# Performance work log

Hardware: AMD Instinct MI355X
Metric: run time of the kernel (lower is better)

## Reference

```python
import jax, jax.numpy as jnp
import numpy as np

B, C, F_IN = 262144, 4, 4   # batch, num label nodes, feature dim
HID = 64                     # hidden_dim (MLP embedding dim / GCN input)
GCN_H, GCN_OUT = 32, 4
EPS = 1e-8                   # torch F.cosine_similarity eps


def _glorot(k, shape):
    lim = float(np.sqrt(6.0 / (shape[0] + shape[1])))
    return jax.random.uniform(k, shape, jnp.float32, -lim, lim)


def setup_inputs() -> dict:
    key = jax.random.key(0)
    ks = jax.random.split(key, 7)
    return dict(
        x=jax.random.normal(ks[0], (B, C, F_IN), jnp.float32),
        # LabelEmbeddingMLP: 4 -> 128 -> 64 -> HID
        W1=_glorot(ks[1], (F_IN, 128)), b1=jnp.zeros((128,), jnp.float32),
        W2=_glorot(ks[2], (128, 64)),   b2=jnp.zeros((64,), jnp.float32),
        W3=_glorot(ks[3], (64, HID)),   b3=jnp.zeros((HID,), jnp.float32),
        # GCNModel: GCNConv(HID,32) -> GCNConv(32,4)
        Wg1=_glorot(ks[4], (HID, GCN_H)), bg1=jnp.zeros((GCN_H,), jnp.float32),
        Wg2=_glorot(ks[5], (GCN_H, GCN_OUT)), bg2=jnp.zeros((GCN_OUT,), jnp.float32),
    )


def reference(x, W1, b1, W2, b2, W3, b3, Wg1, bg1, Wg2, bg2):
    # --- label embedding MLP (applied per node) ---
    h = jax.nn.relu(x @ W1 + b1)
    h = jax.nn.relu(h @ W2 + b2)
    emb = h @ W3 + b3                                    # [B, C, HID]

    # --- per-sample cosine similarity, thresholded, unioned over batch ---
    # (the torch code keeps adding edges to ONE nx.Graph across all k, so the
    #  resulting 4-node edge set is the union over the batch; edge weights are
    #  ignored because GCNConv is called without edge_weight)
    n = x / jnp.maximum(jnp.linalg.norm(x, axis=-1, keepdims=True), EPS)
    sim = jnp.einsum('bif,bjf->bij', n, n)               # [B, C, C]
    adj = (sim > 0.5).any(axis=0) & ~jnp.eye(C, dtype=bool)
    adj = adj | adj.T

    # --- GCN normalized adjacency with self-loops: D^-1/2 (A+I) D^-1/2 ---
    A = adj.astype(jnp.float32) + jnp.eye(C, dtype=jnp.float32)
    dinv = jax.lax.rsqrt(A.sum(axis=1))
    Ahat = jax.lax.stop_gradient(dinv[:, None] * A * dinv[None, :])  # graph built via .item() is detached in torch

    # --- two GCNConv layers, shared Ahat broadcast over batch ---
    g = jax.nn.relu(jnp.einsum('ij,bjh->bih', Ahat, emb @ Wg1) + bg1)  # [B, C, 32]
    out = jnp.einsum('ij,bjh->bih', Ahat, g @ Wg2) + bg2               # [B, C, 4]
    return emb, out
```

## Files before the change

kernel.cpp:

```cpp
#include <hip/hip_runtime.h>

#define NB 262144
#define NNODE (NB * 4)
#define EMB_ELEMS ((size_t)NNODE * 64)
#define ADJ_BLOCKS (NNODE / 256)

typedef __attribute__((ext_vector_type(8))) _Float16 f16x8;
typedef __attribute__((ext_vector_type(4))) float f32x4;
typedef __attribute__((ext_vector_type(4))) unsigned int u32x4;

#define OW1E  0
#define OW2T  10240
#define OW3T  27648
#define OW3GT 36864
#define OF32  41472
#define IMG_BYTES 42880
#define FB2   0
#define FB3   64
#define FB3G  128
#define FBG1  160
#define FWG2  192
#define FBG2  320
#define FAHAT 324

#define NWAVE 8
#define SB_STRIDE 36
#define WBUF_BYTES (64 * SB_STRIDE * 2)
#define SMEM_BYTES (IMG_BYTES + NWAVE * WBUF_BYTES)

__device__ __forceinline__ int kperm(int ji) {
    int kt = ji >> 5, r = ji & 31, g = r >> 3, e = r & 7;
    return kt * 32 + ((e >> 2) << 4) + (g << 2) + (e & 3);
}

template <int J>
__device__ __forceinline__ float qb(float v) {
    constexpr int ctrl = J | (J << 2) | (J << 4) | (J << 6);
    int r = __builtin_amdgcn_update_dpp(0, __builtin_bit_cast(int, v), ctrl, 0xF, 0xF, true);
    return __builtin_bit_cast(float, r);
}

__global__ __launch_bounds__(256) void adj_kernel(const float* __restrict__ x,
                                                  unsigned int* __restrict__ mask_arr) {
    __shared__ unsigned int smask;
    if (threadIdx.x == 0) smask = 0u;
    __syncthreads();

    const int t = blockIdx.x * 256 + threadIdx.x;
    const int c = t & 3;
    f32x4 v = *(const f32x4*)(x + (size_t)t * 4);
    float nn = sqrtf(v.x * v.x + v.y * v.y + v.z * v.z + v.w * v.w);
    float inv = 1.0f / fmaxf(nn, 1e-8f);

    unsigned int m = 0u;
#define DOTJ(J) do {                                                            \
        const float bx = qb<J>(v.x), by = qb<J>(v.y);                           \
        const float bz = qb<J>(v.z), bw = qb<J>(v.w);                           \
        const float bi = qb<J>(inv);                                            \
        const float d = v.x * bx + v.y * by + v.z * bz + v.w * bw;              \
        if ((int)((J) != c) & (int)(d * inv * bi > 0.5f)) {                     \
            const int i_ = c < (J) ? c : (J);                                   \
            const int j_ = c < (J) ? (J) : c;                                   \
            m |= 1u << (2 * i_ + j_ - 1 - (i_ >> 1));                           \
        }                                                                       \
    } while (0)
    DOTJ(0); DOTJ(1); DOTJ(2); DOTJ(3);
#undef DOTJ

    if (m) atomicOr(&smask, m);
    __syncthreads();
    if (threadIdx.x == 0) mask_arr[blockIdx.x] = smask;
}

__global__ __launch_bounds__(256) void prep_kernel(
    const float* __restrict__ W1, const float* __restrict__ b1,
    const float* __restrict__ W2, const float* __restrict__ b2,
    const float* __restrict__ W3, const float* __restrict__ b3,
    const float* __restrict__ Wg1, const float* __restrict__ bg1,
    const float* __restrict__ Wg2, const float* __restrict__ bg2,
    const unsigned int* __restrict__ mask_arr, char* __restrict__ img)
{
    const int t = threadIdx.x;
    const int bid = blockIdx.x;
    _Float16* H = (_Float16*)img;
    float* F = (float*)(img + OF32);

    if (bid == 0) {
        __shared__ unsigned red[256];
        unsigned um = 0u;
        for (int i = t; i < ADJ_BLOCKS; i += 256) um |= mask_arr[i];
        red[t] = um;
        __syncthreads();
        for (int s = 128; s > 0; s >>= 1) {
            if (t < s) red[t] |= red[t + s];
            __syncthreads();
        }
        const unsigned m = red[0];

        for (int i = t; i < 64; i += 256) F[FB2 + i] = b2[i];
        for (int i = t; i < 64; i += 256) F[FB3 + i] = b3[i];
        for (int i = t; i < 32; i += 256) {
            float s = 0.f;
            for (int h = 0; h < 64; ++h) s = fmaf(b3[h], Wg1[h * 32 + i], s);
            F[FB3G + i] = s;
        }
        for (int i = t; i < 32; i += 256) F[FBG1 + i] = bg1[i];
        for (int i = t; i < 128; i += 256) F[FWG2 + i] = Wg2[i];
        for (int i = t; i < 4; i += 256) F[FBG2 + i] = bg2[i];
        if (t == 0) {
            float A[4][4];
            for (int i = 0; i < 4; ++i)
                for (int j = 0; j < 4; ++j) A[i][j] = (i == j) ? 1.f : 0.f;
            int bit = 0;
            for (int i = 0; i < 4; ++i)
                for (int j = i + 1; j < 4; ++j) {
                    if ((m >> bit) & 1u) { A[i][j] = 1.f; A[j][i] = 1.f; }
                    ++bit;
                }
            float dinv[4];
            for (int i = 0; i < 4; ++i)
                dinv[i] = 1.0f / sqrtf(A[i][0] + A[i][1] + A[i][2] + A[i][3]);
            for (int i = 0; i < 4; ++i)
                for (int j = 0; j < 4; ++j) F[FAHAT + i * 4 + j] = dinv[i] * A[i][j] * dinv[j];
        }
    } else if (bid == 1) {
        for (int i = t; i < 128 * 40; i += 256) {
            int j = i / 40, kk = i % 40;
            float v = (kk < 4) ? W1[kk * 128 + j] : (kk == 4 ? b1[j] : 0.f);
            H[OW1E / 2 + i] = (_Float16)v;
        }
    } else if (bid == 2) {
        for (int i = t; i < 64 * 136; i += 256) {
            int jo = i / 136, ji = i % 136;
            float v = 0.f;
            if (ji < 128) v = W2[kperm(ji) * 64 + jo];
            H[OW2T / 2 + i] = (_Float16)v;
        }
    } else {
        for (int i = t; i < 64 * 72; i += 256) {
            int h = i / 72, j = i % 72;
            float v = 0.f;
            if (j < 64) v = W3[kperm(j) * 64 + h];
            H[OW3T / 2 + i] = (_Float16)v;
        }
        for (int i = t; i < 32 * 72; i += 256) {
            int e = i / 72, j = i % 72;
            float s = 0.f;
            if (j < 64) {
                const int jj = kperm(j);
                for (int h = 0; h < 64; ++h) s = fmaf(W3[jj * 64 + h], Wg1[h * 32 + e], s);
            }
            H[OW3GT / 2 + i] = (_Float16)s;
        }
    }
}

__device__ __forceinline__ unsigned pkf16(float a, float b) {
    unsigned short ha = __builtin_bit_cast(unsigned short, (_Float16)a);
    unsigned short hb = __builtin_bit_cast(unsigned short, (_Float16)b);
    return (unsigned)ha | ((unsigned)hb << 16);
}
__device__ __forceinline__ f32x4 MF(f16x8 a, f16x8 b, f32x4 c) {
    return __builtin_amdgcn_mfma_f32_16x16x32_f16(a, b, c, 0, 0, 0);
}
__device__ __forceinline__ f16x8 ldA(const _Float16* p) {
    return *(const f16x8*)p;
}
__device__ __forceinline__ f16x8 bcat(unsigned X0, unsigned X1,
                                      unsigned Y0, unsigned Y1) {
    u32x4 t; t.x = X0; t.y = X1; t.z = Y0; t.w = Y1;
    return __builtin_bit_cast(f16x8, t);
}

__global__ __launch_bounds__(512, 2) void mlp_gcn_mfma(
    const float* __restrict__ x, const char* __restrict__ img,
    float* __restrict__ emb_out, float* __restrict__ out_out)
{
    __shared__ u32x4 smem4[SMEM_BYTES / 16];
    char* smem = (char*)smem4;
    const int tx = threadIdx.x;
    {
        const u32x4* src = (const u32x4*)img;
        u32x4* dst = (u32x4*)smem;
        for (int i = tx; i < IMG_BYTES / 16; i += 512) dst[i] = src[i];
    }
    __syncthreads();

    const _Float16* wh = (const _Float16*)smem;
    const float* wf = (const float*)(smem + OF32);

    const int wid = tx >> 6, lane = tx & 63;
    const int g = lane >> 4, c = lane & 15;
    const bool g0 = (g == 0);

    char* wb = smem + IMG_BYTES + wid * WBUF_BYTES;
    _Float16* sb = (_Float16*)wb;
    float* tb = (float*)wb;

    const f32x4 arow = *(const f32x4*)(wf + FAHAT + (c & 3) * 4);
    f32x4 bg1v[2];
    bg1v[0] = *(const f32x4*)(wf + FBG1 + g * 4);
    bg1v[1] = *(const f32x4*)(wf + FBG1 + 16 + g * 4);
    const f32x4 bg2v = *(const f32x4*)(wf + FBG2);
    f32x4 wg2v[2][4];
#pragma unroll
    for (int m = 0; m < 2; ++m)
#pragma unroll
        for (int r = 0; r < 4; ++r)
            wg2v[m][r] = *(const f32x4*)(wf + FWG2 + (m * 16 + g * 4 + r) * 4);

    const size_t nbase0 = ((size_t)blockIdx.x * NWAVE + wid) * 128;
    f32x4 xv = *(const f32x4*)(x + (nbase0 + lane) * 4);

#pragma unroll 1
    for (int it = 0; it < 2; ++it) {
        const size_t nbase = nbase0 + (size_t)it * 64;
        const size_t pn = (it < 1) ? (nbase + 64) : nbase;
        f32x4 xnext = *(const f32x4*)(x + (pn + lane) * 4);

        {
            uint2 w0; w0.x = pkf16(xv.x, xv.y); w0.y = pkf16(xv.z, xv.w);
            uint2 w1; w1.x = 0x00003C00u; w1.y = 0u;
            *(uint2*)(sb + lane * SB_STRIDE + 0) = w0;
            *(uint2*)(sb + lane * SB_STRIDE + 4) = w1;
        }
        f16x8 xB[4];
#pragma unroll
        for (int nt = 0; nt < 4; ++nt) {
            uint2 lo = *(const uint2*)(sb + (nt * 16 + c) * SB_STRIDE + 0);
            uint2 hi = *(const uint2*)(sb + (nt * 16 + c) * SB_STRIDE + 4);
            u32x4 t;
            t.x = g0 ? lo.x : 0u; t.y = g0 ? lo.y : 0u;
            t.z = g0 ? hi.x : 0u; t.w = 0u;
            xB[nt] = __builtin_bit_cast(f16x8, t);
        }

        f32x4 acc2[4][4];
#pragma unroll
        for (int mt = 0; mt < 4; ++mt) {
            f32x4 bv = *(const f32x4*)(wf + FB2 + mt * 16 + g * 4);
#pragma unroll
            for (int nt = 0; nt < 4; ++nt) acc2[mt][nt] = bv;
        }
#pragma unroll
        for (int kt = 0; kt < 4; ++kt) {
            f16x8 a0 = ldA(wh + OW1E / 2 + ((2 * kt + 0) * 16 + c) * 40 + g * 8);
            f16x8 a1 = ldA(wh + OW1E / 2 + ((2 * kt + 1) * 16 + c) * 40 + g * 8);
            f16x8 bf[4];
#pragma unroll
            for (int nt = 0; nt < 4; ++nt) {
                f32x4 z = {0.f, 0.f, 0.f, 0.f};
                f32x4 t0 = MF(a0, xB[nt], z);
                f32x4 t1 = MF(a1, xB[nt], z);
                bf[nt] = bcat(pkf16(fmaxf(t0[0], 0.f), fmaxf(t0[1], 0.f)),
                              pkf16(fmaxf(t0[2], 0.f), fmaxf(t0[3], 0.f)),
                              pkf16(fmaxf(t1[0], 0.f), fmaxf(t1[1], 0.f)),
                              pkf16(fmaxf(t1[2], 0.f), fmaxf(t1[3], 0.f)));
            }
#pragma unroll
            for (int mt = 0; mt < 4; ++mt) {
                f16x8 a = ldA(wh + OW2T / 2 + (mt * 16 + c) * 136 + kt * 32 + g * 8);
#pragma unroll
                for (int nt = 0; nt < 4; ++nt) acc2[mt][nt] = MF(a, bf[nt], acc2[mt][nt]);
            }
        }

        unsigned pk2a[4][4][2];
#pragma unroll
        for (int mt = 0; mt < 4; ++mt)
#pragma unroll
            for (int nt = 0; nt < 4; ++nt) {
                pk2a[mt][nt][0] = pkf16(fmaxf(acc2[mt][nt][0], 0.f), fmaxf(acc2[mt][nt][1], 0.f));
                pk2a[mt][nt][1] = pkf16(fmaxf(acc2[mt][nt][2], 0.f), fmaxf(acc2[mt][nt][3], 0.f));
            }

        f32x4 acc3[4][4], acc4[2][4];
#pragma unroll
        for (int mt = 0; mt < 4; ++mt) {
            f32x4 bv = *(const f32x4*)(wf + FB3 + mt * 16 + g * 4);
#pragma unroll
            for (int nt = 0; nt < 4; ++nt) acc3[mt][nt] = bv;
        }
#pragma unroll
        for (int mt = 0; mt < 2; ++mt) {
            f32x4 bv = *(const f32x4*)(wf + FB3G + mt * 16 + g * 4);
#pragma unroll
            for (int nt = 0; nt < 4; ++nt) acc4[mt][nt] = bv;
        }
#pragma unroll
        for (int kt = 0; kt < 2; ++kt) {
            f16x8 bf[4];
#pragma unroll
            for (int nt = 0; nt < 4; ++nt)
                bf[nt] = bcat(pk2a[2 * kt][nt][0], pk2a[2 * kt][nt][1],
                              pk2a[2 * kt + 1][nt][0], pk2a[2 * kt + 1][nt][1]);
#pragma unroll
            for (int mt = 0; mt < 4; ++mt) {
                f16x8 a = ldA(wh + OW3T / 2 + (mt * 16 + c) * 72 + kt * 32 + g * 8);
#pragma unroll
                for (int nt = 0; nt < 4; ++nt) acc3[mt][nt] = MF(a, bf[nt], acc3[mt][nt]);
            }
#pragma unroll
            for (int mt = 0; mt < 2; ++mt) {
                f16x8 a = ldA(wh + OW3GT / 2 + (mt * 16 + c) * 72 + kt * 32 + g * 8);
#pragma unroll
                for (int nt = 0; nt < 4; ++nt) acc4[mt][nt] = MF(a, bf[nt], acc4[mt][nt]);
            }
        }

#pragma unroll
        for (int nt = 0; nt < 4; ++nt) {
#pragma unroll
            for (int mt = 0; mt < 4; ++mt) {
                int sl = (mt * 4 + g) ^ (c & 7);
                *(f32x4*)(tb + c * 64 + sl * 4) = acc3[mt][nt];
            }
            float* gp = emb_out + (nbase + nt * 16) * 64;
#pragma unroll
            for (int s = 0; s < 4; ++s) {
                int row = s * 4 + g;
                int sl = c ^ (row & 7);
                f32x4 q = *(const f32x4*)(tb + row * 64 + sl * 4);
                *(f32x4*)(gp + s * 256 + lane * 4) = q;
            }
        }

#pragma unroll
        for (int nt = 0; nt < 4; ++nt) {
            float u[4] = {0.f, 0.f, 0.f, 0.f};
#pragma unroll
            for (int m = 0; m < 2; ++m)
#pragma unroll
                for (int r = 0; r < 4; ++r) {
                    float v = acc4[m][nt][r];
                    float s = bg1v[m][r];
                    s = fmaf(arow.x, qb<0>(v), s);
                    s = fmaf(arow.y, qb<1>(v), s);
                    s = fmaf(arow.z, qb<2>(v), s);
                    s = fmaf(arow.w, qb<3>(v), s);
                    s = fmaxf(s, 0.f);
                    u[0] = fmaf(s, wg2v[m][r].x, u[0]);
                    u[1] = fmaf(s, wg2v[m][r].y, u[1]);
                    u[2] = fmaf(s, wg2v[m][r].z, u[2]);
                    u[3] = fmaf(s, wg2v[m][r].w, u[3]);
                }
#pragma unroll
            for (int o = 0; o < 4; ++o) {
                u[o] += __shfl_xor(u[o], 16);
                u[o] += __shfl_xor(u[o], 32);
            }
            float ov[4];
#pragma unroll
            for (int o = 0; o < 4; ++o) {
                float s = bg2v[o];
                s = fmaf(arow.x, qb<0>(u[o]), s);
                s = fmaf(arow.y, qb<1>(u[o]), s);
                s = fmaf(arow.z, qb<2>(u[o]), s);
                s = fmaf(arow.w, qb<3>(u[o]), s);
                ov[o] = s;
            }
            if (g0) {
                f32x4 t; t.x = ov[0]; t.y = ov[1]; t.z = ov[2]; t.w = ov[3];
                *(f32x4*)(out_out + (nbase + nt * 16 + c) * 4) = t;
            }
        }

        xv = xnext;
    }
}

extern "C" void kernel_launch(void* const* d_in, const int* in_sizes, int n_in,
                              void* d_out, int out_size, void* d_ws, size_t ws_size,
                              hipStream_t stream) {
    const float* x   = (const float*)d_in[0];
    const float* W1  = (const float*)d_in[1];
    const float* b1  = (const float*)d_in[2];
    const float* W2  = (const float*)d_in[3];
    const float* b2  = (const float*)d_in[4];
    const float* W3  = (const float*)d_in[5];
    const float* b3  = (const float*)d_in[6];
    const float* Wg1 = (const float*)d_in[7];
    const float* bg1 = (const float*)d_in[8];
    const float* Wg2 = (const float*)d_in[9];
    const float* bg2 = (const float*)d_in[10];

    unsigned int* mask_arr = (unsigned int*)d_ws;
    char* img = (char*)d_ws + 16640;

    float* emb_out = (float*)d_out;
    float* out_out = emb_out + EMB_ELEMS;

    adj_kernel<<<ADJ_BLOCKS, 256, 0, stream>>>(x, mask_arr);
    prep_kernel<<<4, 256, 0, stream>>>(W1, b1, W2, b2, W3, b3, Wg1, bg1, Wg2, bg2,
                                       mask_arr, img);
    mlp_gcn_mfma<<<NNODE / 1024, 512, 0, stream>>>(x, img, emb_out, out_out);
}
```

Measured before the change: 112.8 us.

## Compute GCN layer-2 projection with MFMA and load x directly into B fragments

Replaces the scalar FMA plus cross-lane shuffle reduction for the second GCN projection (32->4) with a single fp16 MFMA per tile, using a zero-padded, permuted Wg2 fragment precomputed into the shared weight image. The x input is now loaded straight from global memory into the MFMA B operand, dropping the LDS staging buffer and the software prefetch. The emb store loop is moved after the out computation, possibly shortening register live ranges. In exchange it adds fp16 rounding of the GCN hidden activations and gives up the explicit x prefetch.

```diff
diff --git a/kernel.cpp b/kernel.cpp
--- a/kernel.cpp
+++ b/kernel.cpp
@@ -13,19 +13,18 @@
 #define OW2T  10240
 #define OW3T  27648
 #define OW3GT 36864
-#define OF32  41472
-#define IMG_BYTES 42880
+#define OWG2A 41472
+#define OF32  42752
+#define IMG_BYTES 43600
 #define FB2   0
 #define FB3   64
 #define FB3G  128
 #define FBG1  160
-#define FWG2  192
-#define FBG2  320
-#define FAHAT 324
+#define FBG2  192
+#define FAHAT 196
 
 #define NWAVE 8
-#define SB_STRIDE 36
-#define WBUF_BYTES (64 * SB_STRIDE * 2)
+#define WBUF_BYTES 4096
 #define SMEM_BYTES (IMG_BYTES + NWAVE * WBUF_BYTES)
 
 __device__ __forceinline__ int kperm(int ji) {
@@ -105,8 +104,12 @@
             F[FB3G + i] = s;
         }
         for (int i = t; i < 32; i += 256) F[FBG1 + i] = bg1[i];
-        for (int i = t; i < 128; i += 256) F[FWG2 + i] = Wg2[i];
         for (int i = t; i < 4; i += 256) F[FBG2 + i] = bg2[i];
+        for (int i = t; i < 16 * 40; i += 256) {
+            int o = i / 40, ji = i % 40;
+            float v = (o < 4 && ji < 32) ? Wg2[kperm(ji) * 4 + o] : 0.f;
+            H[OWG2A / 2 + i] = (_Float16)v;
+        }
         if (t == 0) {
             float A[4][4];
             for (int i = 0; i < 4; ++i)
@@ -193,45 +196,30 @@
     const int g = lane >> 4, c = lane & 15;
     const bool g0 = (g == 0);
 
-    char* wb = smem + IMG_BYTES + wid * WBUF_BYTES;
-    _Float16* sb = (_Float16*)wb;
-    float* tb = (float*)wb;
+    float* tb = (float*)(smem + IMG_BYTES) + wid * 1024;
 
     const f32x4 arow = *(const f32x4*)(wf + FAHAT + (c & 3) * 4);
     f32x4 bg1v[2];
     bg1v[0] = *(const f32x4*)(wf + FBG1 + g * 4);
     bg1v[1] = *(const f32x4*)(wf + FBG1 + 16 + g * 4);
     const f32x4 bg2v = *(const f32x4*)(wf + FBG2);
-    f32x4 wg2v[2][4];
-#pragma unroll
-    for (int m = 0; m < 2; ++m)
-#pragma unroll
-        for (int r = 0; r < 4; ++r)
-            wg2v[m][r] = *(const f32x4*)(wf + FWG2 + (m * 16 + g * 4 + r) * 4);
+    const f16x8 aWg2 = ldA(wh + OWG2A / 2 + c * 40 + g * 8);
 
     const size_t nbase0 = ((size_t)blockIdx.x * NWAVE + wid) * 128;
-    f32x4 xv = *(const f32x4*)(x + (nbase0 + lane) * 4);
 
 #pragma unroll 1
     for (int it = 0; it < 2; ++it) {
         const size_t nbase = nbase0 + (size_t)it * 64;
-        const size_t pn = (it < 1) ? (nbase + 64) : nbase;
-        f32x4 xnext = *(const f32x4*)(x + (pn + lane) * 4);
-
-        {
-            uint2 w0; w0.x = pkf16(xv.x, xv.y); w0.y = pkf16(xv.z, xv.w);
-            uint2 w1; w1.x = 0x00003C00u; w1.y = 0u;
-            *(uint2*)(sb + lane * SB_STRIDE + 0) = w0;
-            *(uint2*)(sb + lane * SB_STRIDE + 4) = w1;
-        }
+
         f16x8 xB[4];
 #pragma unroll
         for (int nt = 0; nt < 4; ++nt) {
-            uint2 lo = *(const uint2*)(sb + (nt * 16 + c) * SB_STRIDE + 0);
-            uint2 hi = *(const uint2*)(sb + (nt * 16 + c) * SB_STRIDE + 4);
+            f32x4 xq = *(const f32x4*)(x + (nbase + nt * 16 + c) * 4);
             u32x4 t;
-            t.x = g0 ? lo.x : 0u; t.y = g0 ? lo.y : 0u;
-            t.z = g0 ? hi.x : 0u; t.w = 0u;
+            t.x = g0 ? pkf16(xq.x, xq.y) : 0u;
+            t.y = g0 ? pkf16(xq.z, xq.w) : 0u;
+            t.z = g0 ? 0x00003C00u : 0u;
+            t.w = 0u;
             xB[nt] = __builtin_bit_cast(f16x8, t);
         }
 
@@ -310,24 +298,7 @@
 
 #pragma unroll
         for (int nt = 0; nt < 4; ++nt) {
-#pragma unroll
-            for (int mt = 0; mt < 4; ++mt) {
-                int sl = (mt * 4 + g) ^ (c & 7);
-                *(f32x4*)(tb + c * 64 + sl * 4) = acc3[mt][nt];
-            }
-            float* gp = emb_out + (nbase + nt * 16) * 64;
-#pragma unroll
-            for (int s = 0; s < 4; ++s) {
-                int row = s * 4 + g;
-                int sl = c ^ (row & 7);
-                f32x4 q = *(const f32x4*)(tb + row * 64 + sl * 4);
-                *(f32x4*)(gp + s * 256 + lane * 4) = q;
-            }
-        }
-
-#pragma unroll
-        for (int nt = 0; nt < 4; ++nt) {
-            float u[4] = {0.f, 0.f, 0.f, 0.f};
+            float gv[2][4];
 #pragma unroll
             for (int m = 0; m < 2; ++m)
 #pragma unroll
@@ -338,25 +309,20 @@
                     s = fmaf(arow.y, qb<1>(v), s);
                     s = fmaf(arow.z, qb<2>(v), s);
                     s = fmaf(arow.w, qb<3>(v), s);
-                    s = fmaxf(s, 0.f);
-                    u[0] = fmaf(s, wg2v[m][r].x, u[0]);
-                    u[1] = fmaf(s, wg2v[m][r].y, u[1]);
-                    u[2] = fmaf(s, wg2v[m][r].z, u[2]);
-                    u[3] = fmaf(s, wg2v[m][r].w, u[3]);
+                    gv[m][r] = fmaxf(s, 0.f);
                 }
-#pragma unroll
-            for (int o = 0; o < 4; ++o) {
-                u[o] += __shfl_xor(u[o], 16);
-                u[o] += __shfl_xor(u[o], 32);
-            }
+            f16x8 bfg = bcat(pkf16(gv[0][0], gv[0][1]), pkf16(gv[0][2], gv[0][3]),
+                             pkf16(gv[1][0], gv[1][1]), pkf16(gv[1][2], gv[1][3]));
+            f32x4 z = {0.f, 0.f, 0.f, 0.f};
+            f32x4 u4 = MF(aWg2, bfg, z);
             float ov[4];
 #pragma unroll
             for (int o = 0; o < 4; ++o) {
                 float s = bg2v[o];
-                s = fmaf(arow.x, qb<0>(u[o]), s);
-                s = fmaf(arow.y, qb<1>(u[o]), s);
-                s = fmaf(arow.z, qb<2>(u[o]), s);
-                s = fmaf(arow.w, qb<3>(u[o]), s);
+                s = fmaf(arow.x, qb<0>(u4[o]), s);
+                s = fmaf(arow.y, qb<1>(u4[o]), s);
+                s = fmaf(arow.z, qb<2>(u4[o]), s);
+                s = fmaf(arow.w, qb<3>(u4[o]), s);
                 ov[o] = s;
             }
             if (g0) {
@@ -365,7 +331,22 @@
             }
         }
 
-        xv = xnext;
+#pragma unroll
+        for (int nt = 0; nt < 4; ++nt) {
+#pragma unroll
+            for (int mt = 0; mt < 4; ++mt) {
+                int sl = (mt * 4 + g) ^ (c & 7);
+                *(f32x4*)(tb + c * 64 + sl * 4) = acc3[mt][nt];
+            }
+            float* gp = emb_out + (nbase + nt * 16) * 64;
+#pragma unroll
+            for (int s = 0; s < 4; ++s) {
+                int row = s * 4 + g;
+                int sl = c ^ (row & 7);
+                f32x4 q = *(const f32x4*)(tb + row * 64 + sl * 4);
+                *(f32x4*)(gp + s * 256 + lane * 4) = q;
+            }
+        }
     }
 }
 
```

New measurement: 111.8 us. About the same (-0.9%).
